# Kernel tuning notes

Measured on AMD Instinct MI355X. Metric: run time of the kernel, lower is better.

Reference implementation:

```python
import jax, jax.numpy as jnp
import numpy as np

NUM_STEPS = 10
TEMP = 2.0
EPS = 1e-20
K = 4   # number of codebooks
N = 8   # codes per codebook
E = 16  # code dim


def _grid_flat():
    x = np.linspace(0.0, 1.5, NUM_STEPS)
    g = np.stack(np.meshgrid(x, x, x), axis=-1)  # [10,10,10,3], 'xy' indexing as in torch source
    return jnp.asarray(g.reshape(-1, 3), dtype=jnp.float32)  # [1000, 3]


def _gumbel(key, shape):
    u = jax.random.uniform(key, shape, dtype=jnp.float32)
    return -jnp.log(-jnp.log(u + EPS) + EPS)


def setup_inputs() -> dict:
    key = jax.random.key(0)
    k1, k2, k3, k4, k5 = jax.random.split(key, 5)
    B, S, D = 32, 2048, 64
    inputs = jax.random.normal(k1, (B, S, D), dtype=jnp.float32)
    linear_w = jax.random.normal(k2, (64, 3), dtype=jnp.float32) * 0.5
    linear_b = jax.random.normal(k3, (64,), dtype=jnp.float32) * 0.1
    emb = jax.random.normal(k4, (K * N, E), dtype=jnp.float32)
    emb_spaces = emb / jnp.linalg.norm(emb, axis=-1, keepdims=True)  # F.normalize(p=2, dim=-1)
    lin_ws = jax.random.normal(k5, (K, E, D), dtype=jnp.float32) * (1.0 / np.sqrt(D))
    return {"inputs": inputs, "linear_w": linear_w, "linear_b": linear_b,
            "emb_spaces": emb_spaces, "lin_ws": lin_ws}


def reference(inputs, linear_w, linear_b, emb_spaces, lin_ws):
    B, S, D = inputs.shape
    grid = _grid_flat()                       # [1000, 3]
    vecs = grid @ linear_w.T + linear_b       # [1000, 64]

    kc, kp = jax.random.split(jax.random.key(42))

    # ---- coordinate codebook path ----
    xc = jnp.einsum('bsd,nd->bsn', inputs, vecs)          # [B,S,1000]
    logc = jax.nn.log_softmax(xc, axis=-1)
    log_u_c = jnp.log(jnp.float32(1.0 / NUM_STEPS ** 3))
    # KLDivLoss(log_uniform, logc, log_target=True, batchmean with input.size(0)=1) == full sum
    kl_c = jnp.sum(jnp.exp(logc) * (logc - log_u_c))
    ic = jax.nn.softmax((logc + _gumbel(kc, logc.shape)) / TEMP, axis=-1)
    quantized_coord = jnp.einsum('bsn,nd->bsd', ic, vecs)  # [B,S,64]

    # ---- per-codebook path (all 4 codebooks vectorized; nums are uniform = 8) ----
    h = jnp.einsum('bsd,ked->bske', inputs, lin_ws)        # [B,S,K,E]
    embK = emb_spaces.reshape(K, N, E)                     # contiguous slices of emb_spaces
    xp = jnp.einsum('bske,kne->bskn', h, embK)             # [B,S,K,N]
    logp = jax.nn.log_softmax(xp, axis=-1)
    log_u = jnp.log(jnp.float32(1.0 / N))
    kl_p = jnp.sum(jnp.exp(logp) * (logp - log_u))         # sum over the K per-codebook KLs
    ip = jax.nn.softmax((logp + _gumbel(kp, logp.shape)) / TEMP, axis=-1)
    quantized = jnp.einsum('bskn,kne->bske', ip, embK).reshape(B, S, K * E)  # [B,S,64]

    loss = (kl_c + kl_p) / 5.0
    return (quantized, quantized_coord, loss)
```

## Files before the change

### kernel.cpp

```cpp
#include <hip/hip_runtime.h>
#include <cstdint>

#define NROWS_HALF 32768
#define QC_OFF 4194304
#define LOSS_OFF 8388608

#define U_CH 0
#define U_CL 2048
#define WS_LOSS_BYTE 8192

#define X_STRIDE 68
#define LOG2E 1.4426950408889634f
#define LN2   0.6931471805599453f

typedef short short8 __attribute__((ext_vector_type(8)));
typedef float float4v __attribute__((ext_vector_type(4)));

#define MFMA16(a, b, c) __builtin_amdgcn_mfma_f32_16x16x32_bf16((a), (b), (c), 0, 0, 0)

__device__ uint32_t g_ticket;

__host__ __device__ __forceinline__ void tf2x32(uint32_t k0, uint32_t k1,
                                                uint32_t x0, uint32_t x1,
                                                uint32_t& o0, uint32_t& o1) {
  const uint32_t k2 = k0 ^ k1 ^ 0x1BD11BDAu;
#define TF_R(r) { x0 += x1; x1 = (x1 << (r)) | (x1 >> (32 - (r))); x1 ^= x0; }
  x0 += k0; x1 += k1;
  TF_R(13) TF_R(15) TF_R(26) TF_R(6)
  x0 += k1; x1 += k2 + 1u;
  TF_R(17) TF_R(29) TF_R(16) TF_R(24)
  x0 += k2; x1 += k0 + 2u;
  TF_R(13) TF_R(15) TF_R(26) TF_R(6)
  x0 += k0; x1 += k1 + 3u;
  TF_R(17) TF_R(29) TF_R(16) TF_R(24)
  x0 += k1; x1 += k2 + 4u;
  TF_R(13) TF_R(15) TF_R(26) TF_R(6)
  x0 += k2; x1 += k0 + 5u;
#undef TF_R
  o0 = x0; o1 = x1;
}

__device__ __forceinline__ float neglog_u(uint32_t bits) {
  const uint32_t mant = bits >> 9;
  const float u = __uint_as_float(mant | 0x3f800000u) - 1.0f;
  const float delta = (float)(8388608u - mant) * 1.1920928955078125e-7f;
  float nl;
  if (delta < 0.00390625f) {
    nl = delta + 0.5f * delta * delta + 0.33333333f * delta * delta * delta;
  } else {
    nl = -LN2 * __builtin_amdgcn_logf(u + 1e-20f);
  }
  return nl;
}

__device__ __forceinline__ uint32_t rn16(float f) {
  uint32_t u = __float_as_uint(f);
  return (u + 0x7FFFu + ((u >> 16) & 1u)) >> 16;
}

__device__ __forceinline__ void split2_rn(float f0, float f1, uint32_t& hi, uint32_t& lo) {
  uint32_t h0 = rn16(f0), h1 = rn16(f1);
  hi = h0 | (h1 << 16);
  float l0 = f0 - __uint_as_float(h0 << 16);
  float l1 = f1 - __uint_as_float(h1 << 16);
  lo = rn16(l0) | (rn16(l1) << 16);
}

__device__ __forceinline__ void split8_rn(const float* p, short8& hi, short8& lo) {
  float4 f0 = *(const float4*)p;
  float4 f1 = *(const float4*)(p + 4);
  union { uint32_t u[4]; short8 s; } H, L;
  split2_rn(f0.x, f0.y, H.u[0], L.u[0]);
  split2_rn(f0.z, f0.w, H.u[1], L.u[1]);
  split2_rn(f1.x, f1.y, H.u[2], L.u[2]);
  split2_rn(f1.z, f1.w, H.u[3], L.u[3]);
  hi = H.s; lo = L.s;
}

__device__ __forceinline__ short8 as_s8(uint4 v) {
  union { uint4 u; short8 s; } c; c.u = v; return c.s;
}

__device__ __forceinline__ float4v tile_mfma(const ushort* __restrict__ Vh,
                                             const ushort* __restrict__ Vl,
                                             int nb, const short8* ah, const short8* al) {
  uint4 bh0 = *(const uint4*)(Vh + nb);
  uint4 bl0 = *(const uint4*)(Vl + nb);
  float4v acc = {0.f, 0.f, 0.f, 0.f};
  acc = MFMA16(ah[0], as_s8(bh0), acc);
  acc = MFMA16(ah[0], as_s8(bl0), acc);
  acc = MFMA16(al[0], as_s8(bh0), acc);
  uint4 bh1 = *(const uint4*)(Vh + nb + 32);
  uint4 bl1 = *(const uint4*)(Vl + nb + 32);
  acc = MFMA16(ah[1], as_s8(bh1), acc);
  acc = MFMA16(ah[1], as_s8(bl1), acc);
  acc = MFMA16(al[1], as_s8(bh1), acc);
  return acc;
}

__global__ void setup_kernel(const float* __restrict__ emb, const float* __restrict__ lws,
                             ushort* __restrict__ wsu) {
  int idx = blockIdx.x * 256 + threadIdx.x;
  if (idx < 2048) {
    int m = idx >> 6, c = idx & 63, k = m >> 3;
    float a = 0.f;
    #pragma unroll
    for (int e = 0; e < 16; ++e) a += emb[m * 16 + e] * lws[(k * 16 + e) * 64 + c];
    a *= LOG2E;
    uint32_t h = rn16(a);
    float fl = a - __uint_as_float(h << 16);
    wsu[U_CH + idx] = (ushort)h;
    wsu[U_CL + idx] = (ushort)rn16(fl);
  } else if (idx == 2048) {
    *(float*)((char*)wsu + WS_LOSS_BYTE) = 0.f;
    g_ticket = 0u;
  }
}

__global__ __launch_bounds__(256, 4) void fused_kernel(
    const float* __restrict__ inp, const float* __restrict__ emb,
    const float* __restrict__ lw, const float* __restrict__ lb,
    const ushort* __restrict__ wsu, float* __restrict__ out,
    float* __restrict__ loss_acc,
    uint32_t kc0, uint32_t kc1, uint32_t kp0, uint32_t kp1) {

  __shared__ float x_s[16 * X_STRIDE];
  __shared__ float xp_s[16 * 32];
  __shared__ float2 sq2_s[16 * 36];
  __shared__ float u_s[16 * 3];
  __shared__ float swq_s[96];
  __shared__ float tq_s[16 * 4];
  __shared__ float emb_s[512];
  __shared__ float wv_s[512];
  __shared__ float inv_s[64];
  __shared__ float kl_s;

  const int t = threadIdx.x;
  const int lane = t & 63;
  const int w = t >> 6;
  const int q = lane >> 4;
  const int mn = lane & 15;
  const int g0 = blockIdx.x * 8;

  if (t == 0) kl_s = 0.f;

  emb_s[t] = emb[t];
  emb_s[t + 256] = emb[t + 256];

  const float pw0 = lw[lane * 3 + 0];
  const float pw1 = lw[lane * 3 + 1];
  const float pw2 = lw[lane * 3 + 2];

  #pragma unroll
  for (int it = 0; it < 4; ++it) {
    int rl = it * 4 + w;
    int row = (rl < 8) ? (g0 + rl) : (g0 + rl - 8 + NROWS_HALF);
    float v = inp[row * 64 + lane];
    x_s[rl * X_STRIDE + lane] = v;
    float u0 = v * pw0, u1 = v * pw1, u2 = v * pw2;
    #pragma unroll
    for (int off = 32; off > 0; off >>= 1) {
      u0 += __shfl_xor(u0, off);
      u1 += __shfl_xor(u1, off);
      u2 += __shfl_xor(u2, off);
    }
    if (lane == 0) {
      u_s[rl * 3 + 0] = u0; u_s[rl * 3 + 1] = u1; u_s[rl * 3 + 2] = u2;
    }
  }
  __syncthreads();

  if (t < 48) {
    const int row = t & 15, axis = t >> 4;
    const float ua = u_s[row * 3 + axis];
    const float b = 1.5f * fmaxf(ua, 0.f);
    float S = 0.f, W = 0.f;
    #pragma unroll
    for (int i = 0; i < 10; ++i) {
      float gi = (float)(i * (1.5 / 9.0));
      float lg = (ua * gi - b) * LOG2E;
      float P = __builtin_amdgcn_exp2f(lg);
      S += P; W += lg * P;
      sq2_s[row * 36 + axis * 12 + i] = make_float2(__builtin_amdgcn_sqrtf(P), (float)i);
    }
    sq2_s[row * 36 + axis * 12 + 10] = make_float2(0.f, 10.f);
    sq2_s[row * 36 + axis * 12 + 11] = make_float2(0.f, 11.f);
    swq_s[axis * 32 + row * 2 + 0] = S;
    swq_s[axis * 32 + row * 2 + 1] = W;
  }

  short8 ah[2], al[2];
  if (w == 0 || w == 3) {
    #pragma unroll
    for (int s = 0; s < 2; ++s)
      split8_rn(&x_s[mn * X_STRIDE + s * 32 + q * 8], ah[s], al[s]);
  }
  __syncthreads();

  if (t < 16) {
    float Sa = swq_s[t * 2], Wa = swq_s[t * 2 + 1];
    float Sb = swq_s[32 + t * 2], Wb = swq_s[32 + t * 2 + 1];
    float Sc = swq_s[64 + t * 2], Wc = swq_s[64 + t * 2 + 1];
    float kl = LN2 * ((Wa * __builtin_amdgcn_rcpf(Sa) +
                       Wb * __builtin_amdgcn_rcpf(Sb) +
                       Wc * __builtin_amdgcn_rcpf(Sc)) -
                      __builtin_amdgcn_logf(Sa * Sb * Sc)) + 6.9077552789821f;
    atomicAdd(&kl_s, kl);
  }

  if (w == 0 || w == 3) {
    const int cti = (w == 0) ? 1 : 0;
    float4v acc = tile_mfma(wsu + U_CH, wsu + U_CL, (cti * 16 + mn) * 64 + q * 8, ah, al);
    #pragma unroll
    for (int r = 0; r < 4; ++r)
      xp_s[(q * 4 + r) * 32 + cti * 16 + mn] = acc[r];
  }

  float T[16];
  #pragma unroll
  for (int z = 0; z < 16; ++z) T[z] = 0.f;

  #pragma unroll
  for (int pp = 0; pp < 2; ++pp) {
    const int p = w + pp * 4;
    const uint32_t jb = (uint32_t)(g0 + p) * 1000u;
    const float2* sqL = &sq2_s[p * 36];
    const float2* sqH = &sq2_s[(p + 8) * 36];
    float t0l = 0.f, t1l = 0.f, t2l = 0.f, t3l = 0.f;
    float t0h = 0.f, t1h = 0.f, t2h = 0.f, t3h = 0.f;
    #pragma unroll 2
    for (int it = 0; it < 16; ++it) {
      int c = it * 64 + lane;
      uint32_t y0, y1;
      tf2x32(kc0, kc1, jb + (uint32_t)c, jb + (uint32_t)c + 32768000u, y0, y1);
      int d10 = (c * 6554) >> 16;
      int iy  = (c * 656) >> 16;
      int kz  = c - d10 * 10;
      int jx  = d10 - iy * 10;
      float2 a2 = sqL[jx], b2 = sqL[12 + iy], c2 = sqL[24 + kz];
      float2 aH = sqH[jx], bH = sqH[12 + iy], cH = sqH[24 + kz];
      float rL = __builtin_amdgcn_rsqf(neglog_u(y0) + 1e-20f);
      float rH = __builtin_amdgcn_rsqf(neglog_u(y1) + 1e-20f);
      float wL = a2.x * b2.x * (c2.x * rL);
      float wH = aH.x * bH.x * (cH.x * rH);
      t0l += wL; t1l += wL * a2.y; t2l += wL * b2.y; t3l += wL * c2.y;
      t0h += wH; t1h += wH * a2.y; t2h += wH * b2.y; t3h += wH * c2.y;
    }
    T[pp * 8 + 0] = t0l; T[pp * 8 + 1] = t1l; T[pp * 8 + 2] = t2l; T[pp * 8 + 3] = t3l;
    T[pp * 8 + 4] = t0h; T[pp * 8 + 5] = t1h; T[pp * 8 + 6] = t2h; T[pp * 8 + 7] = t3h;
  }

  #pragma unroll
  for (int off = 32; off > 0; off >>= 1) {
    #pragma unroll
    for (int z = 0; z < 16; ++z) T[z] += __shfl_xor(T[z], off);
  }
  if (lane == 0) {
    #pragma unroll
    for (int pp = 0; pp < 2; ++pp) {
      int rl = w + pp * 4, rh = rl + 8;
      #pragma unroll
      for (int cmp = 0; cmp < 4; ++cmp) {
        tq_s[rl * 4 + cmp] = T[pp * 8 + cmp];
        tq_s[rh * 4 + cmp] = T[pp * 8 + 4 + cmp];
      }
    }
  }
  __syncthreads();

  {
    const int d = t & 63, rb = t >> 6;
    const float l0 = lw[d * 3 + 0], l1 = lw[d * 3 + 1], l2 = lw[d * 3 + 2];
    const float lbd = lb[d];
    const float stepf = (float)(1.5 / 9.0);
    #pragma unroll
    for (int kk = 0; kk < 4; ++kk) {
      int m = rb + kk * 4;
      float T0v = tq_s[m * 4 + 0], T1v = tq_s[m * 4 + 1];
      float T2v = tq_s[m * 4 + 2], T3v = tq_s[m * 4 + 3];
      float num = (T1v * l0 + T2v * l1 + T3v * l2) * stepf + T0v * lbd;
      int grow = (m < 8) ? (g0 + m) : (g0 + m - 8 + NROWS_HALF);
      out[QC_OFF + grow * 64 + d] = num * __builtin_amdgcn_rcpf(T0v);
    }
  }

  {
    const int u_ = t >> 3, n = t & 7;
    const int p = u_ >> 2, k = u_ & 3;
    const float xpA = xp_s[p * 32 + k * 8 + n];
    const float xpB = xp_s[(p + 8) * 32 + k * 8 + n];
    float mA = xpA, mB = xpB;
    #pragma unroll
    for (int off = 1; off < 8; off <<= 1) {
      mA = fmaxf(mA, __shfl_xor(mA, off));
      mB = fmaxf(mB, __shfl_xor(mB, off));
    }
    float eA = __builtin_amdgcn_exp2f(xpA - mA);
    float eB = __builtin_amdgcn_exp2f(xpB - mB);
    float s0A = eA, s1A = eA * xpA, s0B = eB, s1B = eB * xpB;
    const uint32_t base = (uint32_t)(g0 + p) * 32u + (uint32_t)k * 8u;
    uint32_t y0, y1;
    tf2x32(kp0, kp1, base + (uint32_t)n, base + (uint32_t)n + 1048576u, y0, y1);
    float wvA = __builtin_amdgcn_exp2f((xpA - mA) * 0.5f) *
                __builtin_amdgcn_rsqf(neglog_u(y0) + 1e-20f);
    float wvB = __builtin_amdgcn_exp2f((xpB - mB) * 0.5f) *
                __builtin_amdgcn_rsqf(neglog_u(y1) + 1e-20f);
    float swA = wvA, swB = wvB;
    #pragma unroll
    for (int off = 1; off < 8; off <<= 1) {
      s0A += __shfl_xor(s0A, off);
      s1A += __shfl_xor(s1A, off);
      s0B += __shfl_xor(s0B, off);
      s1B += __shfl_xor(s1B, off);
      swA += __shfl_xor(swA, off);
      swB += __shfl_xor(swB, off);
    }
    wv_s[u_ * 16 + n] = wvA;
    wv_s[u_ * 16 + 8 + n] = wvB;
    if (n == 0) {
      inv_s[u_ * 2 + 0] = __builtin_amdgcn_rcpf(swA);
      inv_s[u_ * 2 + 1] = __builtin_amdgcn_rcpf(swB);
      atomicAdd(&kl_s,
          LN2 * ((s1A * __builtin_amdgcn_rcpf(s0A) - mA) - __builtin_amdgcn_logf(s0A)) +
          LN2 * ((s1B * __builtin_amdgcn_rcpf(s0B) - mB) - __builtin_amdgcn_logf(s0B)) +
          4.1588830833596715f);
    }
  }
  __syncthreads();

  float* q_s = x_s;
  {
    const int r = t >> 4, e = t & 15;
    const int p = r & 7, h = r >> 3;
    #pragma unroll
    for (int k = 0; k < 4; ++k) {
      const int u_ = p * 4 + k;
      float aa = 0.f;
      #pragma unroll
      for (int n = 0; n < 8; ++n)
        aa += wv_s[u_ * 16 + h * 8 + n] * emb_s[(k * 8 + n) * 16 + e];
      q_s[r * X_STRIDE + k * 16 + e] = aa * inv_s[u_ * 2 + h];
    }
  }
  __syncthreads();

  #pragma unroll
  for (int it = 0; it < 4; ++it) {
    int idx = it * 256 + t;
    int rl = idx >> 6, c = idx & 63;
    int row = (rl < 8) ? (g0 + rl) : (g0 + rl - 8 + NROWS_HALF);
    out[row * 64 + c] = q_s[rl * X_STRIDE + c];
  }
  if (t == 0) {
    atomicAdd(loss_acc, kl_s);
    __threadfence();
    uint32_t tk = atomicAdd(&g_ticket, 1u);
    if (tk == 4095u) {
      __threadfence();
      out[LOSS_OFF] = atomicAdd(loss_acc, 0.0f) * 0.2f;
    }
  }
}

extern "C" void kernel_launch(void* const* d_in, const int* in_sizes, int n_in,
                              void* d_out, int out_size, void* d_ws, size_t ws_size,
                              hipStream_t stream) {
  const float* inp  = (const float*)d_in[0];
  const float* lw   = (const float*)d_in[1];
  const float* lb   = (const float*)d_in[2];
  const float* emb  = (const float*)d_in[3];
  const float* lws  = (const float*)d_in[4];
  float* out = (float*)d_out;
  ushort* wsu = (ushort*)d_ws;
  float* loss = (float*)((char*)d_ws + WS_LOSS_BYTE);

  uint32_t a0, b0, a1, b1;
  tf2x32(0u, 42u, 0u, 2u, a0, b0);
  tf2x32(0u, 42u, 1u, 3u, a1, b1);
  const uint32_t kc0 = a0, kc1 = a1;
  const uint32_t kp0 = b0, kp1 = b1;

  setup_kernel<<<9, 256, 0, stream>>>(emb, lws, wsu);
  fused_kernel<<<4096, 256, 0, stream>>>(inp, emb, lw, lb, wsu, out, loss,
                                         kc0, kc1, kp0, kp1);
}
```

Baseline: 231.8 us.

## Double rows per block, pack paired sq tables into float4, simplify gumbel log

Blocks now have 512 threads and handle 16 row pairs instead of 8. Each pair's low and high rows share one float4 sq table, so the inner loop does three LDS loads where it used to do six. The small-delta Taylor branch in the -log(u) helper is removed and replaced by a direct log2 plus a clamped rsqrt, which shortens the Gumbel path. The risks are lower occupancy from the larger block under launch_bounds(512,4), and small numerical differences for u near 1.

```diff
diff --git a/kernel.cpp b/kernel.cpp
--- a/kernel.cpp
+++ b/kernel.cpp
@@ -40,17 +40,10 @@
   o0 = x0; o1 = x1;
 }
 
-__device__ __forceinline__ float neglog_u(uint32_t bits) {
-  const uint32_t mant = bits >> 9;
-  const float u = __uint_as_float(mant | 0x3f800000u) - 1.0f;
-  const float delta = (float)(8388608u - mant) * 1.1920928955078125e-7f;
-  float nl;
-  if (delta < 0.00390625f) {
-    nl = delta + 0.5f * delta * delta + 0.33333333f * delta * delta * delta;
-  } else {
-    nl = -LN2 * __builtin_amdgcn_logf(u + 1e-20f);
-  }
-  return nl;
+__device__ __forceinline__ float rsq_neglog2(uint32_t bits) {
+  const float u = __uint_as_float((bits >> 9) | 0x3f800000u) - 1.0f;
+  const float l2 = __builtin_amdgcn_logf(u + 1e-20f);
+  return __builtin_amdgcn_rsqf(fmaxf(-l2, 1e-20f));
 }
 
 __device__ __forceinline__ uint32_t rn16(float f) {
@@ -117,22 +110,22 @@
   }
 }
 
-__global__ __launch_bounds__(256, 4) void fused_kernel(
+__global__ __launch_bounds__(512, 4) void fused_kernel(
     const float* __restrict__ inp, const float* __restrict__ emb,
     const float* __restrict__ lw, const float* __restrict__ lb,
     const ushort* __restrict__ wsu, float* __restrict__ out,
     float* __restrict__ loss_acc,
     uint32_t kc0, uint32_t kc1, uint32_t kp0, uint32_t kp1) {
 
-  __shared__ float x_s[16 * X_STRIDE];
-  __shared__ float xp_s[16 * 32];
-  __shared__ float2 sq2_s[16 * 36];
-  __shared__ float u_s[16 * 3];
-  __shared__ float swq_s[96];
-  __shared__ float tq_s[16 * 4];
+  __shared__ float x_s[32 * X_STRIDE];
+  __shared__ float xp_s[32 * 32];
+  __shared__ float4 sq4_s[16 * 3 * 12];
+  __shared__ float u_s[32 * 3];
+  __shared__ float swq_s[192];
+  __shared__ float tq_s[32 * 4];
   __shared__ float emb_s[512];
-  __shared__ float wv_s[512];
-  __shared__ float inv_s[64];
+  __shared__ float wv_s[64 * 16];
+  __shared__ float inv_s[128];
   __shared__ float kl_s;
 
   const int t = threadIdx.x;
@@ -140,12 +133,10 @@
   const int w = t >> 6;
   const int q = lane >> 4;
   const int mn = lane & 15;
-  const int g0 = blockIdx.x * 8;
+  const int g0 = blockIdx.x * 16;
 
   if (t == 0) kl_s = 0.f;
-
   emb_s[t] = emb[t];
-  emb_s[t + 256] = emb[t + 256];
 
   const float pw0 = lw[lane * 3 + 0];
   const float pw1 = lw[lane * 3 + 1];
@@ -153,8 +144,8 @@
 
   #pragma unroll
   for (int it = 0; it < 4; ++it) {
-    int rl = it * 4 + w;
-    int row = (rl < 8) ? (g0 + rl) : (g0 + rl - 8 + NROWS_HALF);
+    int rl = it * 8 + w;
+    int row = (rl < 16) ? (g0 + rl) : (g0 + rl - 16 + NROWS_HALF);
     float v = inp[row * 64 + lane];
     x_s[rl * X_STRIDE + lane] = v;
     float u0 = v * pw0, u1 = v * pw1, u2 = v * pw2;
@@ -170,37 +161,42 @@
   }
   __syncthreads();
 
-  if (t < 48) {
-    const int row = t & 15, axis = t >> 4;
+  if (t < 96) {
+    const int row = t & 31, axis = t >> 5;
+    const int pair = row & 15, half = row >> 4;
     const float ua = u_s[row * 3 + axis];
     const float b = 1.5f * fmaxf(ua, 0.f);
     float S = 0.f, W = 0.f;
+    float2* slotbase = (float2*)&sq4_s[(pair * 3 + axis) * 12];
     #pragma unroll
     for (int i = 0; i < 10; ++i) {
       float gi = (float)(i * (1.5 / 9.0));
       float lg = (ua * gi - b) * LOG2E;
       float P = __builtin_amdgcn_exp2f(lg);
       S += P; W += lg * P;
-      sq2_s[row * 36 + axis * 12 + i] = make_float2(__builtin_amdgcn_sqrtf(P), (float)i);
-    }
-    sq2_s[row * 36 + axis * 12 + 10] = make_float2(0.f, 10.f);
-    sq2_s[row * 36 + axis * 12 + 11] = make_float2(0.f, 11.f);
-    swq_s[axis * 32 + row * 2 + 0] = S;
-    swq_s[axis * 32 + row * 2 + 1] = W;
+      slotbase[i * 2 + half] = make_float2(__builtin_amdgcn_sqrtf(P), (float)i);
+    }
+    slotbase[10 * 2 + half] = make_float2(0.f, 10.f);
+    slotbase[11 * 2 + half] = make_float2(0.f, 11.f);
+    swq_s[axis * 64 + row * 2 + 0] = S;
+    swq_s[axis * 64 + row * 2 + 1] = W;
   }
 
   short8 ah[2], al[2];
-  if (w == 0 || w == 3) {
+  const bool codew = (w < 2) || (w >= 6);
+  const int rt = (w >= 6) ? 1 : 0;
+  const int ct = (w < 2) ? w : (w - 6);
+  if (codew) {
     #pragma unroll
     for (int s = 0; s < 2; ++s)
-      split8_rn(&x_s[mn * X_STRIDE + s * 32 + q * 8], ah[s], al[s]);
-  }
-  __syncthreads();
-
-  if (t < 16) {
-    float Sa = swq_s[t * 2], Wa = swq_s[t * 2 + 1];
-    float Sb = swq_s[32 + t * 2], Wb = swq_s[32 + t * 2 + 1];
-    float Sc = swq_s[64 + t * 2], Wc = swq_s[64 + t * 2 + 1];
+      split8_rn(&x_s[(rt * 16 + mn) * X_STRIDE + s * 32 + q * 8], ah[s], al[s]);
+  }
+  __syncthreads();
+
+  if (t < 32) {
+    float Sa = swq_s[t * 2],       Wa = swq_s[t * 2 + 1];
+    float Sb = swq_s[64 + t * 2],  Wb = swq_s[64 + t * 2 + 1];
+    float Sc = swq_s[128 + t * 2], Wc = swq_s[128 + t * 2 + 1];
     float kl = LN2 * ((Wa * __builtin_amdgcn_rcpf(Sa) +
                        Wb * __builtin_amdgcn_rcpf(Sb) +
                        Wc * __builtin_amdgcn_rcpf(Sc)) -
@@ -208,12 +204,11 @@
     atomicAdd(&kl_s, kl);
   }
 
-  if (w == 0 || w == 3) {
-    const int cti = (w == 0) ? 1 : 0;
-    float4v acc = tile_mfma(wsu + U_CH, wsu + U_CL, (cti * 16 + mn) * 64 + q * 8, ah, al);
+  if (codew) {
+    float4v acc = tile_mfma(wsu + U_CH, wsu + U_CL, (ct * 16 + mn) * 64 + q * 8, ah, al);
     #pragma unroll
     for (int r = 0; r < 4; ++r)
-      xp_s[(q * 4 + r) * 32 + cti * 16 + mn] = acc[r];
+      xp_s[(rt * 16 + q * 4 + r) * 32 + ct * 16 + mn] = acc[r];
   }
 
   float T[16];
@@ -222,10 +217,9 @@
 
   #pragma unroll
   for (int pp = 0; pp < 2; ++pp) {
-    const int p = w + pp * 4;
+    const int p = w + pp * 8;
     const uint32_t jb = (uint32_t)(g0 + p) * 1000u;
-    const float2* sqL = &sq2_s[p * 36];
-    const float2* sqH = &sq2_s[(p + 8) * 36];
+    const float4* base4 = &sq4_s[p * 36];
     float t0l = 0.f, t1l = 0.f, t2l = 0.f, t3l = 0.f;
     float t0h = 0.f, t1h = 0.f, t2h = 0.f, t3h = 0.f;
     #pragma unroll 2
@@ -237,14 +231,13 @@
       int iy  = (c * 656) >> 16;
       int kz  = c - d10 * 10;
       int jx  = d10 - iy * 10;
-      float2 a2 = sqL[jx], b2 = sqL[12 + iy], c2 = sqL[24 + kz];
-      float2 aH = sqH[jx], bH = sqH[12 + iy], cH = sqH[24 + kz];
-      float rL = __builtin_amdgcn_rsqf(neglog_u(y0) + 1e-20f);
-      float rH = __builtin_amdgcn_rsqf(neglog_u(y1) + 1e-20f);
-      float wL = a2.x * b2.x * (c2.x * rL);
-      float wH = aH.x * bH.x * (cH.x * rH);
-      t0l += wL; t1l += wL * a2.y; t2l += wL * b2.y; t3l += wL * c2.y;
-      t0h += wH; t1h += wH * a2.y; t2h += wH * b2.y; t3h += wH * c2.y;
+      float4 a4 = base4[jx], b4 = base4[12 + iy], c4 = base4[24 + kz];
+      float rL = rsq_neglog2(y0);
+      float rH = rsq_neglog2(y1);
+      float wL = a4.x * b4.x * (c4.x * rL);
+      float wH = a4.z * b4.z * (c4.z * rH);
+      t0l += wL; t1l += wL * a4.y; t2l += wL * b4.y; t3l += wL * c4.y;
+      t0h += wH; t1h += wH * a4.y; t2h += wH * b4.y; t3h += wH * c4.y;
     }
     T[pp * 8 + 0] = t0l; T[pp * 8 + 1] = t1l; T[pp * 8 + 2] = t2l; T[pp * 8 + 3] = t3l;
     T[pp * 8 + 4] = t0h; T[pp * 8 + 5] = t1h; T[pp * 8 + 6] = t2h; T[pp * 8 + 7] = t3h;
@@ -258,7 +251,7 @@
   if (lane == 0) {
     #pragma unroll
     for (int pp = 0; pp < 2; ++pp) {
-      int rl = w + pp * 4, rh = rl + 8;
+      int rl = w + pp * 8, rh = rl + 16;
       #pragma unroll
       for (int cmp = 0; cmp < 4; ++cmp) {
         tq_s[rl * 4 + cmp] = T[pp * 8 + cmp];
@@ -275,11 +268,11 @@
     const float stepf = (float)(1.5 / 9.0);
     #pragma unroll
     for (int kk = 0; kk < 4; ++kk) {
-      int m = rb + kk * 4;
+      int m = rb + kk * 8;
       float T0v = tq_s[m * 4 + 0], T1v = tq_s[m * 4 + 1];
       float T2v = tq_s[m * 4 + 2], T3v = tq_s[m * 4 + 3];
       float num = (T1v * l0 + T2v * l1 + T3v * l2) * stepf + T0v * lbd;
-      int grow = (m < 8) ? (g0 + m) : (g0 + m - 8 + NROWS_HALF);
+      int grow = (m < 16) ? (g0 + m) : (g0 + m - 16 + NROWS_HALF);
       out[QC_OFF + grow * 64 + d] = num * __builtin_amdgcn_rcpf(T0v);
     }
   }
@@ -288,7 +281,7 @@
     const int u_ = t >> 3, n = t & 7;
     const int p = u_ >> 2, k = u_ & 3;
     const float xpA = xp_s[p * 32 + k * 8 + n];
-    const float xpB = xp_s[(p + 8) * 32 + k * 8 + n];
+    const float xpB = xp_s[(p + 16) * 32 + k * 8 + n];
     float mA = xpA, mB = xpB;
     #pragma unroll
     for (int off = 1; off < 8; off <<= 1) {
@@ -301,10 +294,8 @@
     const uint32_t base = (uint32_t)(g0 + p) * 32u + (uint32_t)k * 8u;
     uint32_t y0, y1;
     tf2x32(kp0, kp1, base + (uint32_t)n, base + (uint32_t)n + 1048576u, y0, y1);
-    float wvA = __builtin_amdgcn_exp2f((xpA - mA) * 0.5f) *
-                __builtin_amdgcn_rsqf(neglog_u(y0) + 1e-20f);
-    float wvB = __builtin_amdgcn_exp2f((xpB - mB) * 0.5f) *
-                __builtin_amdgcn_rsqf(neglog_u(y1) + 1e-20f);
+    float wvA = __builtin_amdgcn_exp2f((xpA - mA) * 0.5f) * rsq_neglog2(y0);
+    float wvB = __builtin_amdgcn_exp2f((xpB - mB) * 0.5f) * rsq_neglog2(y1);
     float swA = wvA, swB = wvB;
     #pragma unroll
     for (int off = 1; off < 8; off <<= 1) {
@@ -331,7 +322,7 @@
   float* q_s = x_s;
   {
     const int r = t >> 4, e = t & 15;
-    const int p = r & 7, h = r >> 3;
+    const int p = r & 15, h = r >> 4;
     #pragma unroll
     for (int k = 0; k < 4; ++k) {
       const int u_ = p * 4 + k;
@@ -346,16 +337,16 @@
 
   #pragma unroll
   for (int it = 0; it < 4; ++it) {
-    int idx = it * 256 + t;
+    int idx = it * 512 + t;
     int rl = idx >> 6, c = idx & 63;
-    int row = (rl < 8) ? (g0 + rl) : (g0 + rl - 8 + NROWS_HALF);
+    int row = (rl < 16) ? (g0 + rl) : (g0 + rl - 16 + NROWS_HALF);
     out[row * 64 + c] = q_s[rl * X_STRIDE + c];
   }
   if (t == 0) {
     atomicAdd(loss_acc, kl_s);
     __threadfence();
     uint32_t tk = atomicAdd(&g_ticket, 1u);
-    if (tk == 4095u) {
+    if (tk == 2047u) {
       __threadfence();
       out[LOSS_OFF] = atomicAdd(loss_acc, 0.0f) * 0.2f;
     }
@@ -381,6 +372,6 @@
   const uint32_t kp0 = b0, kp1 = b1;
 
   setup_kernel<<<9, 256, 0, stream>>>(emb, lws, wsu);
-  fused_kernel<<<4096, 256, 0, stream>>>(inp, emb, lw, lb, wsu, out, loss,
+  fused_kernel<<<2048, 512, 0, stream>>>(inp, emb, lw, lb, wsu, out, loss,
                                          kc0, kc1, kp0, kp1);
 }
```

After: 219.8 us. -5.2%, faster.
